# Kernel tuning notes

Measured on AMD Instinct MI355X. Metric: run time of the kernel, lower is better.

## Reference

```python
import jax, jax.numpy as jnp
import numpy as np

B, S, D, L = 16, 512, 256, 8192
DROP_P = 0.2


def setup_inputs() -> dict:
    key = jax.random.key(0)
    k1, k2, k3 = jax.random.split(key, 3)
    x = jax.random.normal(k1, (B, S, D), dtype=jnp.float32)
    label_emb = jax.random.normal(k2, (B, L, D), dtype=jnp.float32)
    mask = jax.random.uniform(k3, (B, S)) < 0.9
    return {"x": x, "mask": mask, "label_emb": label_emb}


def reference(x, mask, label_emb):
    # scores = x @ label_emb^T : [B, S, L]
    scores = jnp.einsum("bsd,bld->bsl", x, label_emb)
    # softmax over label dim (last)
    probs = jax.nn.softmax(scores, axis=-1)
    # post-softmax token masking (non-standard order, faithful to original)
    probs = jnp.where(mask[:, :, None], probs, jnp.zeros((), probs.dtype))
    # dropout (training=True in original), deterministic key for reproducibility
    keep = jax.random.bernoulli(jax.random.key(42), 1.0 - DROP_P, probs.shape)
    probs = jnp.where(keep, probs / (1.0 - DROP_P), jnp.zeros((), probs.dtype))
    # attention pooling: scores^T @ x : [B, L, D]
    return jnp.einsum("bsl,bsd->bld", probs, x)
```

## Files before the change

kernel.cpp:

```cpp
#include <hip/hip_runtime.h>
#include <stdint.h>
#include <stddef.h>

#define B_ 16
#define S_ 512
#define D_ 256
#define L_ 8192

typedef unsigned short u16;
typedef _Float16 f16;
typedef f16 f16x4 __attribute__((ext_vector_type(4)));
typedef f16 f16x8 __attribute__((ext_vector_type(8)));
typedef float f32x4 __attribute__((ext_vector_type(4)));

__device__ __forceinline__ void gl16(const void* g, void* l) {
  __builtin_amdgcn_global_load_lds(
      (const __attribute__((address_space(1))) unsigned int*)g,
      (__attribute__((address_space(3))) unsigned int*)l, 16, 0, 0);
}

__device__ __forceinline__ uint32_t rotl32(uint32_t x, int r) {
  return (x << r) | (x >> (32 - r));
}
__device__ __forceinline__ bool drop_keep(uint32_t j) {
  const uint32_t k0 = 0u, k1 = 42u, k2 = 0x1BD11BDAu ^ k0 ^ k1;
  uint32_t v0 = 0u + k0;
  uint32_t v1 = j + k1;
#define TF_R(r) { v0 += v1; v1 = rotl32(v1, (r)); v1 ^= v0; }
  TF_R(13) TF_R(15) TF_R(26) TF_R(6)
  v0 += k1; v1 += k2 + 1u;
  TF_R(17) TF_R(29) TF_R(16) TF_R(24)
  v0 += k2; v1 += k0 + 2u;
  TF_R(13) TF_R(15) TF_R(26) TF_R(6)
  v0 += k0; v1 += k1 + 3u;
  TF_R(17) TF_R(29) TF_R(16) TF_R(24)
  v0 += k1; v1 += k2 + 4u;
  TF_R(13) TF_R(15) TF_R(26) TF_R(6)
  v0 += k2; v1 += k0 + 5u;
#undef TF_R
  uint32_t bits = v0 ^ v1;
  float u = __uint_as_float((bits >> 9) | 0x3f800000u) - 1.0f;
  return u < 0.8f;
}

__global__ __launch_bounds__(256)
void conv16_kernel(const float* __restrict__ src, f16* __restrict__ dst, int n) {
  int i = (blockIdx.x * 256 + threadIdx.x) * 8;
  if (i >= n) return;
  float4 a = *(const float4*)&src[i];
  float4 b = *(const float4*)&src[i + 4];
  f16x8 o;
  o[0] = (f16)a.x; o[1] = (f16)a.y; o[2] = (f16)a.z; o[3] = (f16)a.w;
  o[4] = (f16)b.x; o[5] = (f16)b.y; o[6] = (f16)b.z; o[7] = (f16)b.w;
  *(f16x8*)&dst[i] = o;
}

__global__ __launch_bounds__(256)
void xt16_kernel(const float* __restrict__ x, f16* __restrict__ xT) {
  const int b = blockIdx.z, sb = blockIdx.x * 32, db = blockIdx.y * 32;
  __shared__ float t[32][33];
  const int tid = threadIdx.x;
  const int r = tid >> 3, c4 = (tid & 7) * 4;
  float4 v = *(const float4*)&x[((size_t)b * S_ + sb + r) * D_ + db + c4];
  t[r][c4] = v.x; t[r][c4 + 1] = v.y; t[r][c4 + 2] = v.z; t[r][c4 + 3] = v.w;
  __syncthreads();
  const int dr = tid >> 3, s4 = (tid & 7) * 4;
  f16x4 o;
#pragma unroll
  for (int j = 0; j < 4; ++j) o[j] = (f16)t[s4 + j][dr];
  *(f16x4*)&xT[((size_t)b * D_ + db + dr) * S_ + sb + s4] = o;
}

__global__ __launch_bounds__(256)
void gemm1_f16(const f16* __restrict__ xh, const f16* __restrict__ eh,
               float* __restrict__ scores, float2* __restrict__ partials,
               int s0, int sc) {
  __shared__ __align__(16) f16 As[128 * 32];
  __shared__ __align__(16) f16 Bs[128 * 32];
  __shared__ float pmaxA[128][2];
  __shared__ float psumA[128][2];

  const int tid = threadIdx.x;
  const int lane = tid & 63, wave = tid >> 6;
  const int b = blockIdx.z, lt = blockIdx.x * 128, st = blockIdx.y * 128;

  const int ra = wave * 32 + (lane >> 2);
  const int kc = (lane & 3) * 8;
  const size_t offA0 = ((size_t)b * S_ + s0 + st + ra) * D_ + kc;
  const size_t offA1 = offA0 + 16 * D_;
  const size_t offB0 = ((size_t)b * L_ + lt + ra) * D_ + kc;
  const size_t offB1 = offB0 + 16 * D_;
  const int lo0 = wave * 2048 + lane * 16;

  const int lm = lane & 15, kq = lane >> 4;
  const int wm = (wave & 1) * 64, wn = (wave >> 1) * 64;

  f32x4 acc[4][4] = {};

  for (int k0 = 0; k0 < D_; k0 += 32) {
    __syncthreads();
    gl16(xh + offA0 + k0, (char*)As + lo0);
    gl16(xh + offA1 + k0, (char*)As + lo0 + 1024);
    gl16(eh + offB0 + k0, (char*)Bs + lo0);
    gl16(eh + offB1 + k0, (char*)Bs + lo0 + 1024);
    __syncthreads();

    f16x8 fa[4], fb[4];
#pragma unroll
    for (int mi = 0; mi < 4; ++mi)
      fa[mi] = *(const f16x8*)&As[(wm + mi * 16 + lm) * 32 + kq * 8];
#pragma unroll
    for (int ni = 0; ni < 4; ++ni)
      fb[ni] = *(const f16x8*)&Bs[(wn + ni * 16 + lm) * 32 + kq * 8];
#pragma unroll
    for (int mi = 0; mi < 4; ++mi)
#pragma unroll
      for (int ni = 0; ni < 4; ++ni)
        acc[mi][ni] = __builtin_amdgcn_mfma_f32_16x16x32_f16(
            fa[mi], fb[ni], acc[mi][ni], 0, 0, 0);
  }

#pragma unroll
  for (int mi = 0; mi < 4; ++mi)
#pragma unroll
    for (int ni = 0; ni < 4; ++ni) {
      const int m0 = wm + mi * 16 + kq * 4;
      const int n = wn + ni * 16 + lm;
      float* sp = scores + ((size_t)b * sc + st + m0) * L_ + lt + n;
#pragma unroll
      for (int r = 0; r < 4; ++r) sp[(size_t)r * L_] = acc[mi][ni][r];
    }

  float cmax[4][4];
#pragma unroll
  for (int mi = 0; mi < 4; ++mi)
#pragma unroll
    for (int r = 0; r < 4; ++r) {
      float v = acc[mi][0][r];
      v = fmaxf(v, acc[mi][1][r]);
      v = fmaxf(v, acc[mi][2][r]);
      cmax[mi][r] = fmaxf(v, acc[mi][3][r]);
    }
#pragma unroll
  for (int off = 1; off < 16; off <<= 1)
#pragma unroll
    for (int mi = 0; mi < 4; ++mi)
#pragma unroll
      for (int r = 0; r < 4; ++r)
        cmax[mi][r] = fmaxf(cmax[mi][r], __shfl_xor(cmax[mi][r], off, 64));
  if (lm == 0) {
#pragma unroll
    for (int mi = 0; mi < 4; ++mi)
#pragma unroll
      for (int r = 0; r < 4; ++r)
        pmaxA[wm + mi * 16 + kq * 4 + r][wave >> 1] = cmax[mi][r];
  }
  __syncthreads();
  float rowm[4][4];
#pragma unroll
  for (int mi = 0; mi < 4; ++mi)
#pragma unroll
    for (int r = 0; r < 4; ++r) {
      int row = wm + mi * 16 + kq * 4 + r;
      rowm[mi][r] = fmaxf(pmaxA[row][0], pmaxA[row][1]);
    }
  float psum[4][4] = {};
#pragma unroll
  for (int mi = 0; mi < 4; ++mi)
#pragma unroll
    for (int ni = 0; ni < 4; ++ni)
#pragma unroll
      for (int r = 0; r < 4; ++r)
        psum[mi][r] += __expf(acc[mi][ni][r] - rowm[mi][r]);
#pragma unroll
  for (int off = 1; off < 16; off <<= 1)
#pragma unroll
    for (int mi = 0; mi < 4; ++mi)
#pragma unroll
      for (int r = 0; r < 4; ++r)
        psum[mi][r] += __shfl_xor(psum[mi][r], off, 64);
  if (lm == 0) {
#pragma unroll
    for (int mi = 0; mi < 4; ++mi)
#pragma unroll
      for (int r = 0; r < 4; ++r)
        psumA[wm + mi * 16 + kq * 4 + r][wave >> 1] = psum[mi][r];
  }
  __syncthreads();
  if (tid < 128) {
    float m = fmaxf(pmaxA[tid][0], pmaxA[tid][1]);
    float Z = psumA[tid][0] + psumA[tid][1];
    partials[((size_t)b * 64 + blockIdx.x) * sc + st + tid] = make_float2(m, Z);
  }
}

__global__ __launch_bounds__(256)
void combine_kernel(const float2* __restrict__ partials,
                    const int* __restrict__ mask, float2* __restrict__ stats,
                    int s0, int sc) {
  const int idx = blockIdx.x * 256 + threadIdx.x;
  const int b = idx / sc, si = idx - b * sc;
  float m = -3.402823466e38f, Z = 0.f;
  for (int t = 0; t < 64; ++t) {
    float2 p = partials[((size_t)b * 64 + t) * sc + si];
    if (p.x > m) {
      Z = Z * __expf(m - p.x) + p.y;
      m = p.x;
    } else {
      Z += p.y * __expf(p.x - m);
    }
  }
  float f = (mask[b * S_ + s0 + si] != 0) ? (1.25f / Z) : 0.0f;
  stats[idx] = make_float2(m, f);
}

__global__ __launch_bounds__(256)
void tdrop_kernel(const float* __restrict__ scores,
                  const float2* __restrict__ stats, f16* __restrict__ probsT,
                  int s0, int sc) {
  const int b = blockIdx.z, lt = blockIdx.x * 64, st = blockIdx.y * 64;
  const int tid = threadIdx.x;
  __shared__ float T[64][65];

  const int r0 = tid >> 4, c0 = (tid & 15) * 4;
#pragma unroll
  for (int p = 0; p < 4; ++p) {
    int r = p * 16 + r0;
    float4 v = *(const float4*)&scores[((size_t)b * sc + st + r) * L_ + lt + c0];
    T[r][c0] = v.x; T[r][c0 + 1] = v.y; T[r][c0 + 2] = v.z; T[r][c0 + 3] = v.w;
  }
  __syncthreads();

  const int sb = (tid & 7) * 8;
#pragma unroll
  for (int p = 0; p < 2; ++p) {
    int ll = p * 32 + (tid >> 3);
    f16x8 o;
#pragma unroll
    for (int j = 0; j < 8; ++j) {
      int s_loc = st + sb + j;
      float2 mf = stats[b * sc + s_loc];
      float pv = __expf(T[sb + j][ll] - mf.x) * mf.y;
      uint32_t gidx =
          ((uint32_t)(b * S_ + s0 + s_loc)) * (uint32_t)L_ + (uint32_t)(lt + ll);
      o[j] = drop_keep(gidx) ? (f16)pv : (f16)0.f;
    }
    *(f16x8*)&probsT[((size_t)b * L_ + lt + ll) * S_ + s0 + st + sb] = o;
  }
}

__global__ __launch_bounds__(256)
void gemm2_f16(const f16* __restrict__ pT, const f16* __restrict__ xT,
               float* __restrict__ out) {
  __shared__ __align__(16) f16 As[128 * 32];
  __shared__ __align__(16) f16 Bs[256 * 32];

  const int tid = threadIdx.x;
  const int lane = tid & 63, wave = tid >> 6;
  const int b = blockIdx.z, lt = blockIdx.x * 128;

  const int kc = (lane & 3) * 8;
  const size_t offA0 = ((size_t)b * L_ + lt + wave * 32 + (lane >> 2)) * S_ + kc;
  const size_t offA1 = offA0 + 16 * S_;
  const size_t offB = ((size_t)b * D_ + wave * 64 + (lane >> 2)) * S_ + kc;
  const int loA = wave * 2048 + lane * 16;
  const int loB = wave * 4096 + lane * 16;

  const int lm = lane & 15, kq = lane >> 4;
  const int wm = (wave & 1) * 64, wn = (wave >> 1) * 128;

  f32x4 acc[4][8] = {};

  for (int k0 = 0; k0 < S_; k0 += 32) {
    __syncthreads();
    gl16(pT + offA0 + k0, (char*)As + loA);
    gl16(pT + offA1 + k0, (char*)As + loA + 1024);
#pragma unroll
    for (int i = 0; i < 4; ++i)
      gl16(xT + offB + (size_t)i * 16 * S_ + k0, (char*)Bs + loB + i * 1024);
    __syncthreads();

    f16x8 fa[4], fb[8];
#pragma unroll
    for (int mi = 0; mi < 4; ++mi)
      fa[mi] = *(const f16x8*)&As[(wm + mi * 16 + lm) * 32 + kq * 8];
#pragma unroll
    for (int ni = 0; ni < 8; ++ni)
      fb[ni] = *(const f16x8*)&Bs[(wn + ni * 16 + lm) * 32 + kq * 8];
#pragma unroll
    for (int mi = 0; mi < 4; ++mi)
#pragma unroll
      for (int ni = 0; ni < 8; ++ni)
        acc[mi][ni] = __builtin_amdgcn_mfma_f32_16x16x32_f16(
            fa[mi], fb[ni], acc[mi][ni], 0, 0, 0);
  }

#pragma unroll
  for (int mi = 0; mi < 4; ++mi)
#pragma unroll
    for (int ni = 0; ni < 8; ++ni) {
      const int m0 = wm + mi * 16 + kq * 4;
      const int n = wn + ni * 16 + lm;
      float* op = out + ((size_t)b * L_ + lt + m0) * D_ + n;
#pragma unroll
      for (int r = 0; r < 4; ++r) op[(size_t)r * D_] = acc[mi][ni][r];
    }
}

extern "C" void kernel_launch(void* const* d_in, const int* in_sizes, int n_in,
                              void* d_out, int out_size, void* d_ws, size_t ws_size,
                              hipStream_t stream) {
  const float* x = (const float*)d_in[0];
  const int* mask = (const int*)d_in[1];
  const float* E = (const float*)d_in[2];
  float* out = (float*)d_out;

  char* ws = (char*)d_ws;
  const size_t nE = (size_t)B_ * L_ * D_;
  const size_t nX = (size_t)B_ * S_ * D_;
  size_t o = 0;
  f16* Eh = (f16*)(ws + o); o += nE * 2;
  f16* Xh = (f16*)(ws + o); o += nX * 2;
  f16* XT = (f16*)(ws + o); o += nX * 2;
  float2* stats = (float2*)(ws + o); o += (size_t)B_ * 512 * 8;
  float2* partials = (float2*)(ws + o); o += (size_t)B_ * 64 * 512 * 8;
  const size_t need512 =
      o + (size_t)B_ * 512 * L_ * 4 + (size_t)B_ * L_ * S_ * 2;
  const int sc = (ws_size >= need512) ? 512 : 128;
  float* scores = (float*)(ws + o);
  f16* probsT = (f16*)(ws + o + (size_t)B_ * sc * L_ * 4);

  conv16_kernel<<<dim3((unsigned)(nE / 8 / 256)), 256, 0, stream>>>(E, Eh, (int)nE);
  conv16_kernel<<<dim3((unsigned)(nX / 8 / 256)), 256, 0, stream>>>(x, Xh, (int)nX);
  xt16_kernel<<<dim3(S_ / 32, D_ / 32, B_), 256, 0, stream>>>(x, XT);

  const int nch = S_ / sc;
  for (int c = 0; c < nch; ++c) {
    const int s0 = c * sc;
    gemm1_f16<<<dim3(L_ / 128, sc / 128, B_), 256, 0, stream>>>(
        Xh, Eh, scores, partials, s0, sc);
    combine_kernel<<<dim3(B_ * sc / 256), 256, 0, stream>>>(partials, mask,
                                                            stats, s0, sc);
    tdrop_kernel<<<dim3(L_ / 64, sc / 64, B_), 256, 0, stream>>>(
        scores, stats, probsT, s0, sc);
  }
  gemm2_f16<<<dim3(L_ / 128, 1, B_), 256, 0, stream>>>(probsT, XT, out);
}
```

Before: 598.0 us.

## Fuse softmax-normalize/dropout transpose into second GEMM reading fp32 scores directly

Removes the separate transpose-dropout kernel and the f16 probsT buffer. The second GEMM now loads fp32 score tiles into LDS, applies exp, the softmax stats and the dropout mask on the fly, and feeds the results as MFMA A operands. The block grows to 512 threads, with half the waves loading scores and half loading xT. This saves a full write and read of the transposed probability matrix, but it makes the GEMM load twice the bytes for A (fp32 instead of f16) and recompute the exp and hash per tile. It also drops the chunked fallback for small workspace, so the full scores buffer must always fit.

```diff
diff --git a/kernel.cpp b/kernel.cpp
--- a/kernel.cpp
+++ b/kernel.cpp
@@ -214,97 +214,81 @@
   stats[idx] = make_float2(m, f);
 }
 
-__global__ __launch_bounds__(256)
-void tdrop_kernel(const float* __restrict__ scores,
-                  const float2* __restrict__ stats, f16* __restrict__ probsT,
-                  int s0, int sc) {
-  const int b = blockIdx.z, lt = blockIdx.x * 64, st = blockIdx.y * 64;
-  const int tid = threadIdx.x;
-  __shared__ float T[64][65];
-
-  const int r0 = tid >> 4, c0 = (tid & 15) * 4;
-#pragma unroll
-  for (int p = 0; p < 4; ++p) {
-    int r = p * 16 + r0;
-    float4 v = *(const float4*)&scores[((size_t)b * sc + st + r) * L_ + lt + c0];
-    T[r][c0] = v.x; T[r][c0 + 1] = v.y; T[r][c0 + 2] = v.z; T[r][c0 + 3] = v.w;
-  }
-  __syncthreads();
-
-  const int sb = (tid & 7) * 8;
-#pragma unroll
-  for (int p = 0; p < 2; ++p) {
-    int ll = p * 32 + (tid >> 3);
-    f16x8 o;
-#pragma unroll
-    for (int j = 0; j < 8; ++j) {
-      int s_loc = st + sb + j;
-      float2 mf = stats[b * sc + s_loc];
-      float pv = __expf(T[sb + j][ll] - mf.x) * mf.y;
-      uint32_t gidx =
-          ((uint32_t)(b * S_ + s0 + s_loc)) * (uint32_t)L_ + (uint32_t)(lt + ll);
-      o[j] = drop_keep(gidx) ? (f16)pv : (f16)0.f;
-    }
-    *(f16x8*)&probsT[((size_t)b * L_ + lt + ll) * S_ + s0 + st + sb] = o;
-  }
-}
-
-__global__ __launch_bounds__(256)
-void gemm2_f16(const f16* __restrict__ pT, const f16* __restrict__ xT,
-               float* __restrict__ out) {
-  __shared__ __align__(16) f16 As[128 * 32];
+__global__ __launch_bounds__(512)
+void gemm2_fused(const float* __restrict__ scores, const f16* __restrict__ xT,
+                 const float2* __restrict__ stats, float* __restrict__ out) {
+  __shared__ __align__(16) float Ss[32 * 128];
   __shared__ __align__(16) f16 Bs[256 * 32];
+  __shared__ float2 stat_s[S_];
 
   const int tid = threadIdx.x;
   const int lane = tid & 63, wave = tid >> 6;
   const int b = blockIdx.z, lt = blockIdx.x * 128;
 
-  const int kc = (lane & 3) * 8;
-  const size_t offA0 = ((size_t)b * L_ + lt + wave * 32 + (lane >> 2)) * S_ + kc;
-  const size_t offA1 = offA0 + 16 * S_;
-  const size_t offB = ((size_t)b * D_ + wave * 64 + (lane >> 2)) * S_ + kc;
-  const int loA = wave * 2048 + lane * 16;
-  const int loB = wave * 4096 + lane * 16;
+  stat_s[tid] = stats[b * S_ + tid];
+
+  const int sw = wave & 3;
+  const bool isB = wave >= 4;
+  const size_t sc_base = (size_t)b * S_ * L_ + lt;
+  const size_t xb_base = (size_t)b * D_ * S_;
 
   const int lm = lane & 15, kq = lane >> 4;
-  const int wm = (wave & 1) * 64, wn = (wave >> 1) * 128;
-
-  f32x4 acc[4][8] = {};
+  const int l_loc = wave * 16 + lm;
+  const uint32_t gbase =
+      (uint32_t)(b * S_) * (uint32_t)L_ + (uint32_t)(lt + l_loc);
+
+  f32x4 acc[16] = {};
 
   for (int k0 = 0; k0 < S_; k0 += 32) {
     __syncthreads();
-    gl16(pT + offA0 + k0, (char*)As + loA);
-    gl16(pT + offA1 + k0, (char*)As + loA + 1024);
-#pragma unroll
-    for (int i = 0; i < 4; ++i)
-      gl16(xT + offB + (size_t)i * 16 * S_ + k0, (char*)Bs + loB + i * 1024);
+    if (!isB) {
+#pragma unroll
+      for (int i = 0; i < 4; ++i) {
+        const int c = sw * 4 + i;
+        gl16(scores + sc_base + (size_t)(k0 + 2 * c + (lane >> 5)) * L_ +
+                 (lane & 31) * 4,
+             (char*)Ss + c * 1024);
+      }
+    } else {
+#pragma unroll
+      for (int i = 0; i < 4; ++i) {
+        const int c = sw * 4 + i;
+        gl16(xT + xb_base + (size_t)(c * 16 + (lane >> 2)) * S_ + k0 +
+                 (lane & 3) * 8,
+             (char*)Bs + c * 1024);
+      }
+    }
     __syncthreads();
 
-    f16x8 fa[4], fb[8];
-#pragma unroll
-    for (int mi = 0; mi < 4; ++mi)
-      fa[mi] = *(const f16x8*)&As[(wm + mi * 16 + lm) * 32 + kq * 8];
-#pragma unroll
-    for (int ni = 0; ni < 8; ++ni)
-      fb[ni] = *(const f16x8*)&Bs[(wn + ni * 16 + lm) * 32 + kq * 8];
-#pragma unroll
-    for (int mi = 0; mi < 4; ++mi)
-#pragma unroll
-      for (int ni = 0; ni < 8; ++ni)
-        acc[mi][ni] = __builtin_amdgcn_mfma_f32_16x16x32_f16(
-            fa[mi], fb[ni], acc[mi][ni], 0, 0, 0);
-  }
-
-#pragma unroll
-  for (int mi = 0; mi < 4; ++mi)
-#pragma unroll
-    for (int ni = 0; ni < 8; ++ni) {
-      const int m0 = wm + mi * 16 + kq * 4;
-      const int n = wn + ni * 16 + lm;
-      float* op = out + ((size_t)b * L_ + lt + m0) * D_ + n;
-#pragma unroll
-      for (int r = 0; r < 4; ++r) op[(size_t)r * D_] = acc[mi][ni][r];
-    }
+    float pv[8];
+#pragma unroll
+    for (int j = 0; j < 8; ++j) {
+      const int s_loc = kq * 8 + j;
+      const float sc = Ss[s_loc * 128 + l_loc];
+      const float2 mf = stat_s[k0 + s_loc];
+      pv[j] = __expf(sc - mf.x) * mf.y;
+    }
+    f16x8 fa;
+#pragma unroll
+    for (int j = 0; j < 8; ++j) {
+      const uint32_t gidx = gbase + (uint32_t)(k0 + kq * 8 + j) * (uint32_t)L_;
+      fa[j] = drop_keep(gidx) ? (f16)pv[j] : (f16)0.f;
+    }
+
+#pragma unroll
+    for (int ni = 0; ni < 16; ++ni) {
+      const f16x8 fb = *(const f16x8*)&Bs[(ni * 16 + lm) * 32 + kq * 8];
+      acc[ni] = __builtin_amdgcn_mfma_f32_16x16x32_f16(fa, fb, acc[ni], 0, 0, 0);
+    }
+  }
+
+#pragma unroll
+  for (int ni = 0; ni < 16; ++ni) {
+    const int n = ni * 16 + lm;
+    float* op = out + ((size_t)b * L_ + lt + wave * 16 + kq * 4) * D_ + n;
+#pragma unroll
+    for (int r = 0; r < 4; ++r) op[(size_t)r * D_] = acc[ni][r];
+  }
 }
 
 extern "C" void kernel_launch(void* const* d_in, const int* in_sizes, int n_in,
@@ -322,27 +306,17 @@
   f16* Eh = (f16*)(ws + o); o += nE * 2;
   f16* Xh = (f16*)(ws + o); o += nX * 2;
   f16* XT = (f16*)(ws + o); o += nX * 2;
-  float2* stats = (float2*)(ws + o); o += (size_t)B_ * 512 * 8;
-  float2* partials = (float2*)(ws + o); o += (size_t)B_ * 64 * 512 * 8;
-  const size_t need512 =
-      o + (size_t)B_ * 512 * L_ * 4 + (size_t)B_ * L_ * S_ * 2;
-  const int sc = (ws_size >= need512) ? 512 : 128;
+  float2* stats = (float2*)(ws + o); o += (size_t)B_ * S_ * 8;
+  float2* partials = (float2*)(ws + o); o += (size_t)B_ * 64 * S_ * 8;
   float* scores = (float*)(ws + o);
-  f16* probsT = (f16*)(ws + o + (size_t)B_ * sc * L_ * 4);
 
   conv16_kernel<<<dim3((unsigned)(nE / 8 / 256)), 256, 0, stream>>>(E, Eh, (int)nE);
   conv16_kernel<<<dim3((unsigned)(nX / 8 / 256)), 256, 0, stream>>>(x, Xh, (int)nX);
   xt16_kernel<<<dim3(S_ / 32, D_ / 32, B_), 256, 0, stream>>>(x, XT);
 
-  const int nch = S_ / sc;
-  for (int c = 0; c < nch; ++c) {
-    const int s0 = c * sc;
-    gemm1_f16<<<dim3(L_ / 128, sc / 128, B_), 256, 0, stream>>>(
-        Xh, Eh, scores, partials, s0, sc);
-    combine_kernel<<<dim3(B_ * sc / 256), 256, 0, stream>>>(partials, mask,
-                                                            stats, s0, sc);
-    tdrop_kernel<<<dim3(L_ / 64, sc / 64, B_), 256, 0, stream>>>(
-        scores, stats, probsT, s0, sc);
-  }
-  gemm2_f16<<<dim3(L_ / 128, 1, B_), 256, 0, stream>>>(probsT, XT, out);
-}
+  gemm1_f16<<<dim3(L_ / 128, S_ / 128, B_), 256, 0, stream>>>(
+      Xh, Eh, scores, partials, 0, S_);
+  combine_kernel<<<dim3(B_ * S_ / 256), 256, 0, stream>>>(partials, mask,
+                                                          stats, 0, S_);
+  gemm2_fused<<<dim3(L_ / 128, 1, B_), 512, 0, stream>>>(scores, XT, stats, out);
+}
```

Result: faster. 542.0 us (-9.4%).
